# Kernel optimization log

Hardware: AMD Instinct MI355X
Metric: run time of the kernel (lower is better)

Reference implementation:

```python
import jax, jax.numpy as jnp
import numpy as np

B, T, C, H = 2, 2048, 1024, 16
D = C // H  # head dim = 64

def setup_inputs() -> dict:
    key = jax.random.key(0)
    ks = jax.random.split(key, 5)
    s = 1.0 / np.sqrt(C)
    return {
        "x": jax.random.normal(ks[0], (B, T, C), jnp.float32),
        "Wq": jax.random.normal(ks[1], (C, C), jnp.float32) * s,
        "Wk": jax.random.normal(ks[2], (C, C), jnp.float32) * s,
        "Wv": jax.random.normal(ks[3], (C, C), jnp.float32) * s,
        "Wo": jax.random.normal(ks[4], (C, C), jnp.float32) * s,
    }

def reference(x, Wq, Wk, Wv, Wo):
    # torch Linear: y = x @ W.T  (weights stored [out, in])
    def proj(W):
        h = jnp.einsum('btc,oc->bto', x, W)
        return h.reshape(B, T, H, D).transpose(0, 2, 1, 3)  # [B,H,T,D]
    q, k, v = proj(Wq), proj(Wk), proj(Wv)
    scale = 1.0 / np.sqrt(D)
    att = jnp.einsum('bhqd,bhkd->bhqk', q, k) * scale  # [B,H,T,T]
    causal = jnp.tril(jnp.ones((T, T), bool))
    att = jnp.where(causal[None, None], att, -jnp.inf)
    att = jax.nn.softmax(att, axis=-1)
    y = jnp.einsum('bhqk,bhkd->bhqd', att, v)  # [B,H,T,D]
    y = y.transpose(0, 2, 1, 3).reshape(B, T, C)
    return jnp.einsum('btc,oc->bto', y, Wo)
```

## Files before the change

kernel.cpp:

```cpp
#include <hip/hip_runtime.h>
#include <math.h>

typedef short bf16x8 __attribute__((ext_vector_type(8)));
typedef float f32x4 __attribute__((ext_vector_type(4)));
typedef float f32x16 __attribute__((ext_vector_type(16)));
typedef int int2v __attribute__((ext_vector_type(2)));

constexpr int Bc = 2, Tc = 2048, Cc = 1024, Hc = 16, Dc = 64;
constexpr int Mc = Bc * Tc;

#if __has_builtin(__builtin_amdgcn_exp2f)
#define EXP2(x) __builtin_amdgcn_exp2f(x)
#else
#define EXP2(x) exp2f(x)
#endif

#define SBAR() do { asm volatile("" ::: "memory"); \
                    __builtin_amdgcn_s_barrier();   \
                    asm volatile("" ::: "memory"); } while (0)

__device__ __forceinline__ unsigned short f2bf(float f) {
    union { float f; unsigned u; } v; v.f = f;
    unsigned r = v.u + 0x7fffu + ((v.u >> 16) & 1u);
    return (unsigned short)(r >> 16);
}

__device__ __forceinline__ float bf2f(unsigned short u) {
    union { unsigned u; float f; } v; v.u = (unsigned)u << 16; return v.f;
}

__device__ __forceinline__ unsigned cvt_pk_bf16(float lo, float hi) {
    unsigned r;
    asm("v_cvt_pk_bf16_f32 %0, %1, %2" : "=v"(r) : "v"(lo), "v"(hi));
    return r;
}

__device__ __forceinline__ void gload16(const void* g, void* l) {
    __builtin_amdgcn_global_load_lds(
        (const __attribute__((address_space(1))) void*)g,
        (__attribute__((address_space(3))) void*)l, 16, 0, 0);
}

__global__ __launch_bounds__(256)
void cast_bf16(const float* __restrict__ in, unsigned short* __restrict__ out, int n8) {
    int i = blockIdx.x * 256 + threadIdx.x;
    if (i >= n8) return;
    const float4* p = (const float4*)in;
    float4 a = p[i * 2], b = p[i * 2 + 1];
    union { unsigned short u[8]; bf16x8 v; } r;
    r.u[0] = f2bf(a.x); r.u[1] = f2bf(a.y); r.u[2] = f2bf(a.z); r.u[3] = f2bf(a.w);
    r.u[4] = f2bf(b.x); r.u[5] = f2bf(b.y); r.u[6] = f2bf(b.z); r.u[7] = f2bf(b.w);
    *(bf16x8*)(out + i * 8) = r.v;
}

__global__ __launch_bounds__(256)
void cast_w4(const float* __restrict__ a, const float* __restrict__ b,
             const float* __restrict__ c, const float* __restrict__ d,
             unsigned short* __restrict__ oa, unsigned short* __restrict__ ob,
             unsigned short* __restrict__ oc, unsigned short* __restrict__ od) {
    const float* src = blockIdx.y == 0 ? a : blockIdx.y == 1 ? b : blockIdx.y == 2 ? c : d;
    unsigned short* dst = blockIdx.y == 0 ? oa : blockIdx.y == 1 ? ob : blockIdx.y == 2 ? oc : od;
    int i = blockIdx.x * 256 + threadIdx.x;
    const float4* p = (const float4*)src;
    float4 x = p[i * 2], y = p[i * 2 + 1];
    union { unsigned short u[8]; bf16x8 v; } r;
    r.u[0] = f2bf(x.x); r.u[1] = f2bf(x.y); r.u[2] = f2bf(x.z); r.u[3] = f2bf(x.w);
    r.u[4] = f2bf(y.x); r.u[5] = f2bf(y.y); r.u[6] = f2bf(y.z); r.u[7] = f2bf(y.w);
    *(bf16x8*)(dst + i * 8) = r.v;
}

__global__ __launch_bounds__(256)
void gemm_qkv(const unsigned short* __restrict__ A,
              const unsigned short* __restrict__ Wq,
              const unsigned short* __restrict__ Wk,
              const unsigned short* __restrict__ Wv,
              unsigned short* __restrict__ Qo,
              unsigned short* __restrict__ Ko,
              unsigned short* __restrict__ Vo) {
    __shared__ unsigned short As[128 * 32];
    __shared__ unsigned short Bs[64 * 32];
    const int t = threadIdx.x;
    const int lane = t & 63, l15 = lane & 15, l4 = lane >> 4;
    const int w = t >> 6, wr = w >> 1, wc = w & 1;
    const int seg = blockIdx.y >> 4;
    const unsigned short* W = seg == 0 ? Wq : seg == 1 ? Wk : Wv;
    const int m0 = blockIdx.x * 128, n0 = (blockIdx.y & 15) * 64;

    f32x4 acc[4][2] = {};

    for (int k0 = 0; k0 < Cc; k0 += 32) {
        __syncthreads();
        #pragma unroll
        for (int it = 0; it < 2; ++it) {
            int c = t + it * 256;
            int row = c >> 2, ko = (c & 3) << 3;
            gload16(A + (size_t)(m0 + row) * Cc + k0 + ko, As + c * 8);
        }
        {
            int row = t >> 2, ko = (t & 3) << 3;
            gload16(W + (size_t)(n0 + row) * Cc + k0 + ko, Bs + t * 8);
        }
        __syncthreads();
        bf16x8 af[4], bfr[2];
        #pragma unroll
        for (int i = 0; i < 4; ++i)
            af[i] = *(const bf16x8*)(As + ((wr * 64 + i * 16 + l15) * 32 + l4 * 8));
        #pragma unroll
        for (int j = 0; j < 2; ++j)
            bfr[j] = *(const bf16x8*)(Bs + ((wc * 32 + j * 16 + l15) * 32 + l4 * 8));
        #pragma unroll
        for (int i = 0; i < 4; ++i)
            #pragma unroll
            for (int j = 0; j < 2; ++j)
                acc[i][j] = __builtin_amdgcn_mfma_f32_16x16x32_bf16(af[i], bfr[j], acc[i][j], 0, 0, 0);
    }

    const float qscale = 0.18033688011112042f;
    const int r0 = wr * 64 + (l4 << 2);
    const int c0 = wc * 32 + l15;
    #pragma unroll
    for (int i = 0; i < 4; ++i)
        #pragma unroll
        for (int j = 0; j < 2; ++j)
            #pragma unroll
            for (int r = 0; r < 4; ++r) {
                int row = m0 + r0 + i * 16 + r;
                int col = n0 + c0 + j * 16;
                float v = acc[i][j][r];
                int bb = row >> 11, tt = row & (Tc - 1);
                int hh = col >> 6, dd = col & 63;
                if (seg == 0)
                    Qo[((((size_t)bb * Hc + hh) * Tc + tt) << 6) + dd] = f2bf(v * qscale);
                else if (seg == 1)
                    Ko[((((size_t)bb * Hc + hh) * Tc + tt) << 6) + dd] = f2bf(v);
                else
                    Vo[(((size_t)bb * Hc + hh) * Dc + dd) * Tc + tt] = f2bf(v);
            }
}

__global__ __launch_bounds__(256)
void gemm_out(const unsigned short* __restrict__ A,
              const unsigned short* __restrict__ W,
              float* __restrict__ outp) {
    __shared__ unsigned short As[64 * 32];
    __shared__ unsigned short Bs[64 * 32];
    const int t = threadIdx.x;
    const int lane = t & 63, l15 = lane & 15, l4 = lane >> 4;
    const int w = t >> 6, wr = w >> 1, wc = w & 1;
    const int m0 = blockIdx.x * 64, n0 = blockIdx.y * 64;

    f32x4 acc[2][2] = {};

    for (int k0 = 0; k0 < Cc; k0 += 32) {
        __syncthreads();
        {
            int row = t >> 2, ko = (t & 3) << 3;
            gload16(A + (size_t)(m0 + row) * Cc + k0 + ko, As + t * 8);
            gload16(W + (size_t)(n0 + row) * Cc + k0 + ko, Bs + t * 8);
        }
        __syncthreads();
        bf16x8 af[2], bfr[2];
        #pragma unroll
        for (int i = 0; i < 2; ++i)
            af[i] = *(const bf16x8*)(As + ((wr * 32 + i * 16 + l15) * 32 + l4 * 8));
        #pragma unroll
        for (int j = 0; j < 2; ++j)
            bfr[j] = *(const bf16x8*)(Bs + ((wc * 32 + j * 16 + l15) * 32 + l4 * 8));
        #pragma unroll
        for (int i = 0; i < 2; ++i)
            #pragma unroll
            for (int j = 0; j < 2; ++j)
                acc[i][j] = __builtin_amdgcn_mfma_f32_16x16x32_bf16(af[i], bfr[j], acc[i][j], 0, 0, 0);
    }

    const int r0 = wr * 32 + (l4 << 2);
    const int c0 = wc * 32 + l15;
    #pragma unroll
    for (int i = 0; i < 2; ++i)
        #pragma unroll
        for (int j = 0; j < 2; ++j)
            #pragma unroll
            for (int r = 0; r < 4; ++r)
                outp[(size_t)(m0 + r0 + i * 16 + r) * Cc + n0 + c0 + j * 16] = acc[i][j][r];
}

__device__ __constant__ unsigned char JOBS[48] = {
    159, 223, 222, 15, 158, 157, 221, 220, 14, 156,
    155, 219, 218, 13, 154, 153, 217, 216, 12, 152,
    151, 215, 214, 11, 150, 149, 213, 212, 10, 148,
    147, 211, 210,  9, 146, 145, 209, 208,  8, 144,
      7,   6,   5,  4,   3,   2,   1,   0
};

__global__ __launch_bounds__(128)
void attn_mfma(const unsigned short* __restrict__ Q,
               const unsigned short* __restrict__ K,
               const unsigned short* __restrict__ Vt,
               unsigned short* __restrict__ Y,
               unsigned short* __restrict__ P1,
               float* __restrict__ mlf) {
    __shared__ unsigned short Ks[2][64 * 64];
    __shared__ unsigned short Vs[2][64 * 64];

    const int t = threadIdx.x, lane = t & 63, w = t >> 6;
    const int l31 = lane & 31, h = lane >> 5;
    const int bh = blockIdx.x;
    const int bb = bh >> 4, hh = bh & 15;

    const unsigned char job = JOBS[blockIdx.y];
    const int c = job & 31;
    const bool split = job & 128;
    const int half = (job >> 6) & 1;
    const int ntile = c + 1, smid = ntile >> 1;
    const int kb0 = (split && half) ? smid : 0;
    const int kb1 = (split && !half) ? smid : ntile;

    const int qbase = c * 64 + w * 32;
    const int q = qbase + l31;

    const unsigned short* Qp = Q + (size_t)bh * Tc * Dc;
    const unsigned short* Kp = K + (size_t)bh * Tc * Dc;
    const unsigned short* Vp = Vt + (size_t)bh * Dc * Tc;

    bf16x8 qf[4];
    #pragma unroll
    for (int kc = 0; kc < 4; ++kc)
        qf[kc] = *(const bf16x8*)(Qp + (size_t)q * 64 + kc * 16 + h * 8);

    f32x16 ot[2] = {};
    float m = -INFINITY, lsum = 0.f;

    auto stage = [&](int kb, int buf) {
        #pragma unroll
        for (int it = 0; it < 4; ++it) {
            int idx = t + it * 128;
            int row = idx >> 3, slot = idx & 7;
            int ss = slot ^ (row & 7);
            gload16(Kp + (size_t)(kb * 64 + row) * 64 + ss * 8, &Ks[buf][idx * 8]);
            gload16(Vp + (size_t)row * Tc + kb * 64 + ss * 8, &Vs[buf][idx * 8]);
        }
    };

    stage(kb0, 0);
    if (kb0 + 1 < kb1) stage(kb0 + 1, 1);

    for (int kb = kb0; kb < kb1; ++kb) {
        const int cur = (kb - kb0) & 1;
        if (kb + 1 < kb1) asm volatile("s_waitcnt vmcnt(8)" ::: "memory");
        else              asm volatile("s_waitcnt vmcnt(0)" ::: "memory");
        SBAR();

        f32x16 st[2] = {};
        __builtin_amdgcn_s_setprio(1);
        #pragma unroll
        for (int nt = 0; nt < 2; ++nt) {
            int key = nt * 32 + l31;
            #pragma unroll
            for (int kc = 0; kc < 4; ++kc) {
                int boff = (kc * 32 + h * 16) ^ ((key & 7) << 4);
                bf16x8 kf = *(const bf16x8*)(&Ks[cur][((key << 7) + boff) >> 1]);
                st[nt] = __builtin_amdgcn_mfma_f32_32x32x16_bf16(kf, qf[kc], st[nt], 0, 0, 0);
            }
        }
        __builtin_amdgcn_s_setprio(0);

        if (kb * 64 + 63 > qbase) {
            #pragma unroll
            for (int nt = 0; nt < 2; ++nt)
                #pragma unroll
                for (int r = 0; r < 16; ++r) {
                    int key = kb * 64 + nt * 32 + (r & 3) + 8 * (r >> 2) + 4 * h;
                    if (key > q) st[nt][r] = -1e30f;
                }
        }

        float mx[16];
        #pragma unroll
        for (int r = 0; r < 16; ++r) mx[r] = fmaxf(st[0][r], st[1][r]);
        #pragma unroll
        for (int s2 = 8; s2 > 0; s2 >>= 1)
            #pragma unroll
            for (int r = 0; r < s2; ++r) mx[r] = fmaxf(mx[r], mx[r + s2]);
        float tmax = fmaxf(mx[0], __shfl_xor(mx[0], 32));

        if (__any(tmax > m + 8.f)) {
            float mn = fmaxf(m, tmax);
            float al = EXP2(m - mn);
            m = mn;
            lsum *= al;
            #pragma unroll
            for (int dt = 0; dt < 2; ++dt)
                #pragma unroll
                for (int r = 0; r < 16; ++r) ot[dt][r] *= al;
        }

        float psa[4] = {0.f, 0.f, 0.f, 0.f};
        #pragma unroll
        for (int nt = 0; nt < 2; ++nt)
            #pragma unroll
            for (int r = 0; r < 16; ++r) {
                float p = EXP2(st[nt][r] - m);
                st[nt][r] = p;
                psa[r & 3] += p;
            }
        lsum += (psa[0] + psa[1]) + (psa[2] + psa[3]);

        #pragma unroll
        for (int nt = 0; nt < 2; ++nt) {
            unsigned a0 = cvt_pk_bf16(st[nt][0],  st[nt][1]);
            unsigned b0 = cvt_pk_bf16(st[nt][4],  st[nt][5]);
            unsigned a1 = cvt_pk_bf16(st[nt][2],  st[nt][3]);
            unsigned b1 = cvt_pk_bf16(st[nt][6],  st[nt][7]);
            int2v r0 = __builtin_amdgcn_permlane32_swap((int)a0, (int)b0, false, false);
            int2v r1 = __builtin_amdgcn_permlane32_swap((int)a1, (int)b1, false, false);
            union { unsigned u[4]; bf16x8 v; } pf0, pf1;
            pf0.u[0] = r0.x; pf0.u[1] = r1.x; pf0.u[2] = r0.y; pf0.u[3] = r1.y;
            unsigned c0 = cvt_pk_bf16(st[nt][8],  st[nt][9]);
            unsigned d0 = cvt_pk_bf16(st[nt][12], st[nt][13]);
            unsigned c1 = cvt_pk_bf16(st[nt][10], st[nt][11]);
            unsigned d1 = cvt_pk_bf16(st[nt][14], st[nt][15]);
            int2v r2 = __builtin_amdgcn_permlane32_swap((int)c0, (int)d0, false, false);
            int2v r3 = __builtin_amdgcn_permlane32_swap((int)c1, (int)d1, false, false);
            pf1.u[0] = r2.x; pf1.u[1] = r3.x; pf1.u[2] = r2.y; pf1.u[3] = r3.y;

            __builtin_amdgcn_s_setprio(1);
            #pragma unroll
            for (int dt = 0; dt < 2; ++dt) {
                int d = dt * 32 + l31;
                int v0off = (nt * 64 + h * 16) ^ ((d & 7) << 4);
                bf16x8 vf0 = *(const bf16x8*)(&Vs[cur][((d << 7) + v0off) >> 1]);
                ot[dt] = __builtin_amdgcn_mfma_f32_32x32x16_bf16(vf0, pf0.v, ot[dt], 0, 0, 0);
            }
            #pragma unroll
            for (int dt = 0; dt < 2; ++dt) {
                int d = dt * 32 + l31;
                int v1off = (nt * 64 + 32 + h * 16) ^ ((d & 7) << 4);
                bf16x8 vf1 = *(const bf16x8*)(&Vs[cur][((d << 7) + v1off) >> 1]);
                ot[dt] = __builtin_amdgcn_mfma_f32_32x32x16_bf16(vf1, pf1.v, ot[dt], 0, 0, 0);
            }
            __builtin_amdgcn_s_setprio(0);
        }

        SBAR();
        if (kb + 2 < kb1) stage(kb + 2, cur);
    }

    float lf = lsum + __shfl_xor(lsum, 32);
    unsigned short* dst = (split && half) ? P1 : Y;
    float inv = split ? 1.f : 1.f / lf;
    size_t base = ((size_t)bb * Tc + q) * Cc + hh * 64;
    #pragma unroll
    for (int dt = 0; dt < 2; ++dt)
        #pragma unroll
        for (int rg = 0; rg < 4; ++rg) {
            int d0 = dt * 32 + rg * 8 + 4 * h;
            ushort4 s4;
            s4.x = f2bf(ot[dt][rg * 4 + 0] * inv);
            s4.y = f2bf(ot[dt][rg * 4 + 1] * inv);
            s4.z = f2bf(ot[dt][rg * 4 + 2] * inv);
            s4.w = f2bf(ot[dt][rg * 4 + 3] * inv);
            *(ushort4*)(dst + base + d0) = s4;
        }
    if (split && h == 0) {
        int ridx = bh * 1024 + (q - 1024);
        mlf[ridx + (half ? 65536 : 0)]     = m;
        mlf[ridx + (half ? 98304 : 32768)] = lf;
    }
}

__global__ __launch_bounds__(256)
void attn_combine(unsigned short* __restrict__ Y,
                  const unsigned short* __restrict__ P1,
                  const float* __restrict__ mlf) {
    int tid = blockIdx.x * 256 + threadIdx.x;
    int ridx = tid >> 3;
    int d0 = (tid & 7) * 8;
    int bh = ridx >> 10, qq = ridx & 1023;
    int bb = bh >> 4, hh = bh & 15;
    int q = 1024 + qq;
    size_t off = ((size_t)bb * Tc + q) * Cc + hh * 64 + d0;
    float m0 = mlf[ridx], l0 = mlf[ridx + 32768];
    float m1 = mlf[ridx + 65536], l1 = mlf[ridx + 98304];
    float M = fmaxf(m0, m1);
    float a0 = exp2f(m0 - M), a1 = exp2f(m1 - M);
    float inv = 1.f / (l0 * a0 + l1 * a1);
    union { unsigned short u[8]; bf16x8 v; } y0, y1, r;
    y0.v = *(const bf16x8*)(Y + off);
    y1.v = *(const bf16x8*)(P1 + off);
    #pragma unroll
    for (int j = 0; j < 8; ++j)
        r.u[j] = f2bf((bf2f(y0.u[j]) * a0 + bf2f(y1.u[j]) * a1) * inv);
    *(bf16x8*)(Y + off) = r.v;
}

extern "C" void kernel_launch(void* const* d_in, const int* in_sizes, int n_in,
                              void* d_out, int out_size, void* d_ws, size_t ws_size,
                              hipStream_t stream) {
    const float* x  = (const float*)d_in[0];
    const float* Wq = (const float*)d_in[1];
    const float* Wk = (const float*)d_in[2];
    const float* Wv = (const float*)d_in[3];
    const float* Wo = (const float*)d_in[4];

    unsigned short* ws = (unsigned short*)d_ws;
    const size_t nX = (size_t)Mc * Cc;
    const size_t nW = (size_t)Cc * Cc;
    size_t off = 0;
    unsigned short* xb  = ws + off; off += nX;
    unsigned short* Wqb = ws + off; off += nW;
    unsigned short* Wkb = ws + off; off += nW;
    unsigned short* Wvb = ws + off; off += nW;
    unsigned short* Wob = ws + off; off += nW;
    unsigned short* Qw  = ws + off; off += nX;
    unsigned short* Kw  = ws + off; off += nX;
    unsigned short* Vtw = ws + off; off += nX;
    unsigned short* Yb  = ws + off; off += nX;

    dim3 blk(256);
    cast_bf16<<<dim3((int)(nX / 8 / 256)), blk, 0, stream>>>(x, xb, (int)(nX / 8));
    cast_w4<<<dim3(512, 4), blk, 0, stream>>>(Wq, Wk, Wv, Wo, Wqb, Wkb, Wvb, Wob);

    gemm_qkv<<<dim3(Mc / 128, 48), blk, 0, stream>>>(xb, Wqb, Wkb, Wvb, Qw, Kw, Vtw);

    unsigned short* P1 = xb;
    float* mlf = (float*)Wqb;
    attn_mfma<<<dim3(Bc * Hc, 48), dim3(128), 0, stream>>>(Qw, Kw, Vtw, Yb, P1, mlf);
    attn_combine<<<dim3(1024), blk, 0, stream>>>(Yb, P1, mlf);

    gemm_out<<<dim3(Mc / 64, Cc / 64), blk, 0, stream>>>(Yb, Wob, (float*)d_out);
}
```

Baseline: 133.3 us.

## Widen QKV GEMM tile to 128x128 and load V fragments directly from global

The QKV projection GEMM now uses 128-column output tiles per block: each block computes a 128x128 tile with 16 accumulators per wave, and the grid halves along y. This reuses each A tile across twice as many columns. In attention, V is no longer staged through shared memory. Each lane loads its V fragments straight from global memory into registers at the start of every key block, and the async wait count is adjusted to match. This cuts LDS traffic and footprint, but V loads now sit on the critical path without double buffering, and register pressure rises in both kernels.

```diff
diff --git a/kernel.cpp b/kernel.cpp
--- a/kernel.cpp
+++ b/kernel.cpp
@@ -78,15 +78,15 @@
               unsigned short* __restrict__ Ko,
               unsigned short* __restrict__ Vo) {
     __shared__ unsigned short As[128 * 32];
-    __shared__ unsigned short Bs[64 * 32];
+    __shared__ unsigned short Bs[128 * 32];
     const int t = threadIdx.x;
     const int lane = t & 63, l15 = lane & 15, l4 = lane >> 4;
     const int w = t >> 6, wr = w >> 1, wc = w & 1;
-    const int seg = blockIdx.y >> 4;
+    const int seg = blockIdx.y >> 3;
     const unsigned short* W = seg == 0 ? Wq : seg == 1 ? Wk : Wv;
-    const int m0 = blockIdx.x * 128, n0 = (blockIdx.y & 15) * 64;
-
-    f32x4 acc[4][2] = {};
+    const int m0 = blockIdx.x * 128, n0 = (blockIdx.y & 7) * 128;
+
+    f32x4 acc[4][4] = {};
 
     for (int k0 = 0; k0 < Cc; k0 += 32) {
         __syncthreads();
@@ -95,33 +95,30 @@
             int c = t + it * 256;
             int row = c >> 2, ko = (c & 3) << 3;
             gload16(A + (size_t)(m0 + row) * Cc + k0 + ko, As + c * 8);
-        }
-        {
-            int row = t >> 2, ko = (t & 3) << 3;
-            gload16(W + (size_t)(n0 + row) * Cc + k0 + ko, Bs + t * 8);
+            gload16(W + (size_t)(n0 + row) * Cc + k0 + ko, Bs + c * 8);
         }
         __syncthreads();
-        bf16x8 af[4], bfr[2];
+        bf16x8 af[4], bfr[4];
         #pragma unroll
         for (int i = 0; i < 4; ++i)
             af[i] = *(const bf16x8*)(As + ((wr * 64 + i * 16 + l15) * 32 + l4 * 8));
         #pragma unroll
-        for (int j = 0; j < 2; ++j)
-            bfr[j] = *(const bf16x8*)(Bs + ((wc * 32 + j * 16 + l15) * 32 + l4 * 8));
+        for (int j = 0; j < 4; ++j)
+            bfr[j] = *(const bf16x8*)(Bs + ((wc * 64 + j * 16 + l15) * 32 + l4 * 8));
         #pragma unroll
         for (int i = 0; i < 4; ++i)
             #pragma unroll
-            for (int j = 0; j < 2; ++j)
+            for (int j = 0; j < 4; ++j)
                 acc[i][j] = __builtin_amdgcn_mfma_f32_16x16x32_bf16(af[i], bfr[j], acc[i][j], 0, 0, 0);
     }
 
     const float qscale = 0.18033688011112042f;
     const int r0 = wr * 64 + (l4 << 2);
-    const int c0 = wc * 32 + l15;
+    const int c0 = wc * 64 + l15;
     #pragma unroll
     for (int i = 0; i < 4; ++i)
         #pragma unroll
-        for (int j = 0; j < 2; ++j)
+        for (int j = 0; j < 4; ++j)
             #pragma unroll
             for (int r = 0; r < 4; ++r) {
                 int row = m0 + r0 + i * 16 + r;
@@ -200,7 +197,6 @@
                unsigned short* __restrict__ P1,
                float* __restrict__ mlf) {
     __shared__ unsigned short Ks[2][64 * 64];
-    __shared__ unsigned short Vs[2][64 * 64];
 
     const int t = threadIdx.x, lane = t & 63, w = t >> 6;
     const int l31 = lane & 31, h = lane >> 5;
@@ -230,25 +226,35 @@
     f32x16 ot[2] = {};
     float m = -INFINITY, lsum = 0.f;
 
-    auto stage = [&](int kb, int buf) {
+    auto stageK = [&](int kb, int buf) {
         #pragma unroll
         for (int it = 0; it < 4; ++it) {
             int idx = t + it * 128;
             int row = idx >> 3, slot = idx & 7;
             int ss = slot ^ (row & 7);
             gload16(Kp + (size_t)(kb * 64 + row) * 64 + ss * 8, &Ks[buf][idx * 8]);
-            gload16(Vp + (size_t)row * Tc + kb * 64 + ss * 8, &Vs[buf][idx * 8]);
         }
     };
 
-    stage(kb0, 0);
-    if (kb0 + 1 < kb1) stage(kb0 + 1, 1);
+    stageK(kb0, 0);
+    if (kb0 + 1 < kb1) stageK(kb0 + 1, 1);
 
     for (int kb = kb0; kb < kb1; ++kb) {
         const int cur = (kb - kb0) & 1;
-        if (kb + 1 < kb1) asm volatile("s_waitcnt vmcnt(8)" ::: "memory");
+        if (kb + 1 < kb1) asm volatile("s_waitcnt vmcnt(4)" ::: "memory");
         else              asm volatile("s_waitcnt vmcnt(0)" ::: "memory");
         SBAR();
+
+        bf16x8 vf[2][2][2];
+        #pragma unroll
+        for (int nt = 0; nt < 2; ++nt)
+            #pragma unroll
+            for (int ks = 0; ks < 2; ++ks)
+                #pragma unroll
+                for (int dt = 0; dt < 2; ++dt)
+                    vf[nt][ks][dt] = *(const bf16x8*)(
+                        Vp + (size_t)(dt * 32 + l31) * Tc
+                           + kb * 64 + nt * 32 + ks * 16 + h * 8);
 
         f32x16 st[2] = {};
         __builtin_amdgcn_s_setprio(1);
@@ -325,24 +331,16 @@
 
             __builtin_amdgcn_s_setprio(1);
             #pragma unroll
-            for (int dt = 0; dt < 2; ++dt) {
-                int d = dt * 32 + l31;
-                int v0off = (nt * 64 + h * 16) ^ ((d & 7) << 4);
-                bf16x8 vf0 = *(const bf16x8*)(&Vs[cur][((d << 7) + v0off) >> 1]);
-                ot[dt] = __builtin_amdgcn_mfma_f32_32x32x16_bf16(vf0, pf0.v, ot[dt], 0, 0, 0);
-            }
-            #pragma unroll
-            for (int dt = 0; dt < 2; ++dt) {
-                int d = dt * 32 + l31;
-                int v1off = (nt * 64 + 32 + h * 16) ^ ((d & 7) << 4);
-                bf16x8 vf1 = *(const bf16x8*)(&Vs[cur][((d << 7) + v1off) >> 1]);
-                ot[dt] = __builtin_amdgcn_mfma_f32_32x32x16_bf16(vf1, pf1.v, ot[dt], 0, 0, 0);
-            }
+            for (int dt = 0; dt < 2; ++dt)
+                ot[dt] = __builtin_amdgcn_mfma_f32_32x32x16_bf16(vf[nt][0][dt], pf0.v, ot[dt], 0, 0, 0);
+            #pragma unroll
+            for (int dt = 0; dt < 2; ++dt)
+                ot[dt] = __builtin_amdgcn_mfma_f32_32x32x16_bf16(vf[nt][1][dt], pf1.v, ot[dt], 0, 0, 0);
             __builtin_amdgcn_s_setprio(0);
         }
 
         SBAR();
-        if (kb + 2 < kb1) stage(kb + 2, cur);
+        if (kb + 2 < kb1) stageK(kb + 2, cur);
     }
 
     float lf = lsum + __shfl_xor(lsum, 32);
@@ -420,7 +418,7 @@
     cast_bf16<<<dim3((int)(nX / 8 / 256)), blk, 0, stream>>>(x, xb, (int)(nX / 8));
     cast_w4<<<dim3(512, 4), blk, 0, stream>>>(Wq, Wk, Wv, Wo, Wqb, Wkb, Wvb, Wob);
 
-    gemm_qkv<<<dim3(Mc / 128, 48), blk, 0, stream>>>(xb, Wqb, Wkb, Wvb, Qw, Kw, Vtw);
+    gemm_qkv<<<dim3(Mc / 128, 24), blk, 0, stream>>>(xb, Wqb, Wkb, Wvb, Qw, Kw, Vtw);
 
     unsigned short* P1 = xb;
     float* mlf = (float*)Wqb;
```

New measurement: 123.2 us. 7.6% less time.
